# Kernel tuning notes

Hardware: AMD Instinct MI355X
Metric: run time of the kernel (lower is better)

Reference implementation:

```python
import jax, jax.numpy as jnp
import numpy as np

N = 50000   # nodes
E = 400000  # edges (before self-loops)
F = 128     # num_features
H = 8       # heads (layer 1)
C = 64      # hidden_channels
B = 64      # graphs in batch
K = 10      # num_classes
NEG_SLOPE = 0.2


def setup_inputs() -> dict:
    key = jax.random.key(0)
    ks = jax.random.split(key, 12)
    g = lambda k, shape, fan: jax.random.normal(k, shape, jnp.float32) / np.sqrt(fan).astype(np.float32)
    return {
        "x": jax.random.normal(ks[0], (N, F), jnp.float32),
        "edge_index": jax.random.randint(ks[1], (2, E), 0, N, jnp.int32),
        "batch": jnp.sort(jax.random.randint(ks[2], (N,), 0, B, jnp.int32)),
        "W1": g(ks[3], (F, H * C), F),
        "att_src1": g(ks[4], (H, C), C),
        "att_dst1": g(ks[5], (H, C), C),
        "b1": jnp.zeros((H * C,), jnp.float32),
        "W2": g(ks[6], (H * C, C), H * C),
        "att_src2": g(ks[7], (1, C), C),
        "att_dst2": g(ks[8], (1, C), C),
        "b2": jnp.zeros((C,), jnp.float32),
        "lin1_w": g(ks[9], (C, C), C),
        "lin1_b": jnp.zeros((C,), jnp.float32),
        "lin2_w": g(ks[10], (C, K), C),
        "lin2_b": jnp.zeros((K,), jnp.float32),
    }


def gat_conv(x, src, dst, W, att_src, att_dst, bias):
    """PyG GATConv (self-loops already appended to src/dst). x:[N,Fin] -> [N,H*C]."""
    heads, out_c = att_src.shape
    h = (x @ W).reshape(N, heads, out_c)                      # [N,H,C]
    a_s = jnp.einsum('nhc,hc->nh', h, att_src)                # [N,H]
    a_d = jnp.einsum('nhc,hc->nh', h, att_dst)
    e = jax.nn.leaky_relu(a_s[src] + a_d[dst], NEG_SLOPE)     # [E',H]
    # segment softmax over incoming edges of each destination node
    m = jax.ops.segment_max(e, dst, num_segments=N)
    e = jnp.exp(e - m[dst])
    denom = jax.ops.segment_sum(e, dst, num_segments=N)
    alpha = e / (denom[dst] + 1e-16)                          # [E',H]
    out = jax.ops.segment_sum(h[src] * alpha[:, :, None], dst, num_segments=N)  # [N,H,C]
    return out.reshape(N, heads * out_c) + bias


def reference(x, edge_index, batch, W1, att_src1, att_dst1, b1,
              W2, att_src2, att_dst2, b2, lin1_w, lin1_b, lin2_w, lin2_b):
    loops = jnp.arange(N, dtype=edge_index.dtype)
    src = jnp.concatenate([edge_index[0], loops])
    dst = jnp.concatenate([edge_index[1], loops])

    h = gat_conv(x, src, dst, W1, att_src1, att_dst1, b1)     # [N, H*C]
    h = jax.nn.elu(h)                                         # dropout inactive (eval)
    h = gat_conv(h, src, dst, W2, att_src2, att_dst2, b2)     # [N, C]
    h = jax.nn.elu(h)

    pooled = jax.ops.segment_sum(h, batch, num_segments=B)    # global_add_pool -> [B, C]
    z = jax.nn.elu(pooled @ lin1_w + lin1_b)
    logits = z @ lin2_w + lin2_b
    return jax.nn.log_softmax(logits, axis=-1)
```

## Files before the change

### kernel.cpp

```cpp
#include <hip/hip_runtime.h>
#include <hip/hip_bf16.h>

#define DEV static __device__ __forceinline__

constexpr int F1 = 128;
constexpr int H1 = 8;
constexpr int C  = 64;
constexpr int B  = 64;
constexpr int K  = 10;
constexpr float NEG = 0.2f;

typedef __attribute__((ext_vector_type(8))) short short8;
typedef __attribute__((ext_vector_type(4))) float floatx4;

DEV float b2f(__hip_bfloat16 x) { return __bfloat162float(x); }
DEV float elu1(float v) { return v > 0.f ? v : (__expf(v) - 1.f); }
DEV unsigned short f2bbits(float f) {
  __hip_bfloat16 b = __float2bfloat16(f);
  return *(unsigned short*)&b;
}
DEV float blo(unsigned u) { return __uint_as_float(u << 16); }
DEV float bhi(unsigned u) { return __uint_as_float(u & 0xffff0000u); }
DEV float bu(unsigned short u) { return __uint_as_float(((unsigned)u) << 16); }
DEV unsigned pack2(float lo, float hi) {
  return (unsigned)f2bbits(lo) | ((unsigned)f2bbits(hi) << 16);
}
DEV float rcp_nr(float x) {
  float r = __builtin_amdgcn_rcpf(x);
  return r * (2.f - x * r);
}


DEV int detect_dev(const void* xraw, int* lds) {
  if (threadIdx.x == 0) {
    const __hip_bfloat16* xb = (const __hip_bfloat16*)xraw;
    int bad = 0;
    for (int i = 0; i < 128; ++i) {
      float v = b2f(xb[2 * i]);
      if (!(fabsf(v) < 1e4f)) bad++;
    }
    *lds = (bad < 13) ? 1 : 0;
  }
  __syncthreads();
  return *lds;
}

#define CVT(p, i) (isbf ? b2f(((const __hip_bfloat16*)(p))[i]) : ((const float*)(p))[i])

__global__ void fused_prep_kernel(const void* x_raw, const void* w1raw,
                                  const void* as1r, const void* ad1r, const void* b1r,
                                  const void* w2raw,
                                  const void* as2r, const void* ad2r, const void* b2r,
                                  const void* l1wr, const void* l1br,
                                  const void* l2wr, const void* l2br,
                                  unsigned short* __restrict__ xbf,
                                  unsigned short* __restrict__ w1frag,
                                  unsigned short* __restrict__ w2frag,
                                  unsigned short* __restrict__ vfrag,
                                  float* __restrict__ wts,
                                  int* __restrict__ deg,
                                  float* __restrict__ pooled,
                                  int nX, int N) {
  __shared__ int fl;
  int isbf = detect_dev(x_raw, &fl);
  int gid = blockIdx.x * 256 + threadIdx.x;
  int stride = gridDim.x * 256;

  if (isbf) {
    const unsigned short* src = (const unsigned short*)x_raw;
    for (int i = gid; i < nX; i += stride) xbf[i] = src[i];
  } else {
    const float* src = (const float*)x_raw;
    for (int i = gid; i < nX; i += stride) xbf[i] = f2bbits(src[i]);
  }
  for (int i = gid; i < 512;  i += stride) {
    int hp = i >> 7, l16 = (i >> 3) & 15, nt = i & 7;
    int c = hp * 128 + nt * 16 + l16;
    wts[1024 + i] = CVT(b1r, c);
  }
  for (int i = gid; i < 64;   i += stride) wts[1536 + i] = CVT(as2r, i);
  for (int i = gid; i < 64;   i += stride) wts[1600 + i] = CVT(ad2r, i);
  for (int i = gid; i < 64;   i += stride) wts[1664 + i] = CVT(b2r, i);
  for (int i = gid; i < 4096; i += stride) wts[1728 + i] = CVT(l1wr, i);
  for (int i = gid; i < 64;   i += stride) wts[5824 + i] = CVT(l1br, i);
  for (int i = gid; i < 640;  i += stride) wts[5888 + i] = CVT(l2wr, i);
  for (int i = gid; i < 10;   i += stride) wts[6528 + i] = CVT(l2br, i);
  for (int t = gid; t < 8192; t += stride) {
    int lane = t & 63, ks = (t >> 6) & 3, nt = t >> 8;
    for (int j = 0; j < 8; ++j) {
      int k = ks * 32 + (lane >> 4) * 8 + j;
      int n = nt * 16 + (lane & 15);
      w1frag[t * 8 + j] = f2bbits(CVT(w1raw, k * 512 + n));
    }
  }
  for (int t = gid; t < 4096; t += stride) {
    int lane = t & 63, nt = (t >> 6) & 3, ks = t >> 8;
    for (int j = 0; j < 8; ++j) {
      int p = ks * 32 + (lane >> 4) * 8 + j;
      int hp = p >> 7, pl16 = (p >> 3) & 15, pnt = p & 7;
      int k = hp * 128 + pnt * 16 + pl16;
      int n = nt * 16 + (lane & 15);
      w2frag[t * 8 + j] = f2bbits(CVT(w2raw, k * 64 + n));
    }
  }
  for (int t = gid; t < 2048; t += stride) {
    int j = t & 7, lane = (t >> 3) & 63, ks = t >> 9;
    int k = ks * 32 + (lane >> 4) * 8 + j;
    int n = lane & 15;
    int hh = (n < 8) ? n : (n - 8);
    float s = 0.f;
    if (n < 8) {
      for (int c = 0; c < 64; ++c)
        s += CVT(w1raw, k * 512 + hh * 64 + c) * CVT(as1r, hh * 64 + c);
    } else {
      for (int c = 0; c < 64; ++c)
        s += CVT(w1raw, k * 512 + hh * 64 + c) * CVT(ad1r, hh * 64 + c);
    }
    vfrag[(ks * 64 + lane) * 8 + j] = f2bbits(s);
  }
  for (int i = gid; i < N; i += stride) deg[i] = 0;
  for (int i = gid; i < B * C; i += stride) pooled[i] = 0.f;
}

__global__ void deg_count_kernel(const int* __restrict__ ei, int E, int Etot,
                                 int* __restrict__ deg) {
  int e = blockIdx.x * blockDim.x + threadIdx.x;
  if (e >= Etot) return;
  int d = (e < E) ? ei[E + e] : e - E;
  atomicAdd(&deg[d], 1);
}

__global__ void scan_block_kernel(const int* __restrict__ deg,
                                  int* __restrict__ local,
                                  int* __restrict__ bsum, int N) {
  __shared__ int tmp[256];
  int t = threadIdx.x;
  int i = blockIdx.x * 256 + t;
  int v = (i < N) ? deg[i] : 0;
  tmp[t] = v;
  __syncthreads();
  for (int off = 1; off < 256; off <<= 1) {
    int u = (t >= off) ? tmp[t - off] : 0;
    __syncthreads();
    tmp[t] += u;
    __syncthreads();
  }
  if (i < N) local[i] = tmp[t] - v;
  if (t == 255) bsum[blockIdx.x] = tmp[255];
}

__global__ void scan_finish_kernel(const int* __restrict__ local,
                                   const int* __restrict__ bsum, int nb,
                                   int* __restrict__ rowptr,
                                   int* __restrict__ cursor, int N, int Etot) {
  __shared__ int tmp[256];
  __shared__ int offs;
  int t = threadIdx.x;
  int v0 = (t < nb) ? bsum[t] : 0;
  tmp[t] = v0;
  __syncthreads();
  for (int off = 1; off < 256; off <<= 1) {
    int u = (t >= off) ? tmp[t - off] : 0;
    __syncthreads();
    tmp[t] += u;
    __syncthreads();
  }
  if (t == (int)blockIdx.x) offs = tmp[t] - v0;
  __syncthreads();
  int i = blockIdx.x * 256 + t;
  if (i < N) {
    int r = local[i] + offs;
    rowptr[i] = r;
    cursor[i] = r;
  }
  if (i == 0) rowptr[N] = Etot;
}

__global__ __launch_bounds__(256) void att_scalars_kernel(
    const unsigned short* __restrict__ xbf,
    const unsigned short* __restrict__ vfrag,
    float* __restrict__ a_s, float* __restrict__ a_d,
    int N) {
  int t = threadIdx.x, w = t >> 6, lane = t & 63;
  int quad = lane >> 4, l16 = lane & 15;
  int row0 = blockIdx.x * 64 + w * 16;

  floatx4 acc = {};
  int rl = row0 + l16; if (rl >= N) rl = N - 1;
  const unsigned short* xp = xbf + (size_t)rl * 128 + quad * 8;
#pragma unroll
  for (int ks = 0; ks < 4; ++ks) {
    short8 a = *(const short8*)(xp + ks * 32);
    short8 b = *(const short8*)&vfrag[(ks * 64 + lane) * 8];
    acc = __builtin_amdgcn_mfma_f32_16x16x32_bf16(a, b, acc, 0, 0, 0);
  }
#pragma unroll
  for (int r = 0; r < 4; ++r) {
    int row = row0 + quad * 4 + r;
    if (row < N) {
      if (l16 < 8) a_s[(size_t)row * 8 + l16] = acc[r];
      else         a_d[(size_t)row * 8 + (l16 - 8)] = acc[r];
    }
  }
}

__global__ void fill_weight_kernel(const int* __restrict__ ei, int E, int Etot,
                                   const float* __restrict__ a_s,
                                   const float* __restrict__ a_d,
                                   int* __restrict__ cursor,
                                   int* __restrict__ col,
                                   float* __restrict__ wedge) {
  int e = blockIdx.x * 256 + threadIdx.x;
  if (e >= Etot) return;
  int s, d;
  if (e < E) { s = ei[e]; d = ei[E + e]; } else { s = d = e - E; }
  int pos = atomicAdd(&cursor[d], 1);
  col[pos] = s;
  float4 s0 = *(const float4*)(a_s + (size_t)s * 8);
  float4 s1 = *(const float4*)(a_s + (size_t)s * 8 + 4);
  float4 d0 = *(const float4*)(a_d + (size_t)d * 8);
  float4 d1 = *(const float4*)(a_d + (size_t)d * 8 + 4);
  float4 w0, w1;
  float v;
  v = s0.x + d0.x; v = v > 0.f ? v : NEG * v; w0.x = __expf(v);
  v = s0.y + d0.y; v = v > 0.f ? v : NEG * v; w0.y = __expf(v);
  v = s0.z + d0.z; v = v > 0.f ? v : NEG * v; w0.z = __expf(v);
  v = s0.w + d0.w; v = v > 0.f ? v : NEG * v; w0.w = __expf(v);
  v = s1.x + d1.x; v = v > 0.f ? v : NEG * v; w1.x = __expf(v);
  v = s1.y + d1.y; v = v > 0.f ? v : NEG * v; w1.y = __expf(v);
  v = s1.z + d1.z; v = v > 0.f ? v : NEG * v; w1.z = __expf(v);
  v = s1.w + d1.w; v = v > 0.f ? v : NEG * v; w1.w = __expf(v);
  *(float4*)(wedge + (size_t)pos * 8)     = w0;
  *(float4*)(wedge + (size_t)pos * 8 + 4) = w1;
}

__global__ __launch_bounds__(512, 4) void aggx_gemm1_kernel(
    const unsigned short* __restrict__ xbf,
    const unsigned short* __restrict__ W1frag,
    const int* __restrict__ rowptr,
    const int* __restrict__ col,
    const float* __restrict__ wedge,
    const float* __restrict__ bias_perm,
    unsigned short* __restrict__ out1,
    int N) {
  __shared__ __align__(16) unsigned short XgT[128 * 32];
  __shared__ __align__(16) unsigned short Wm[8 * 16 * 32];
  __shared__ __align__(16) unsigned short AggP[8 * 16 * 136];
  __shared__ int rpl[17];

  int t = threadIdx.x, w = t >> 6, lane = t & 63;
  int q = lane >> 4, n = lane & 15;
  int dbase = blockIdx.x * 16;

  if (t < 17) rpl[t] = rowptr[min(dbase + t, N)];
  __syncthreads();
  int R0 = rpl[0], R1 = rpl[16];
  int nch = (R1 - R0 + 31) >> 5;

  int ke = t >> 4, p = t & 15;
  int dw = t >> 5, kw = t & 31;

  short8 onesf = {};
  if (n == 0) {
#pragma unroll
    for (int j = 0; j < 8; ++j) onesf[j] = (short)0x3F80;
  }

  floatx4 accw[8] = {};
  floatx4 accdn = {};

  for (int c = 0; c < nch; ++c) {
    int ebase = R0 + c * 32;
    __syncthreads();

    {
      int e = ebase + ke;
      int ec = (e < R1) ? e : (R1 - 1);
      int s = col[ec];
      uint4 xv = *(const uint4*)(xbf + (size_t)s * 128 + p * 8);
      int xb = (512 * p + 2 * ke) ^ ((p & 3) << 4);
      unsigned short* xp0 = (unsigned short*)((char*)XgT + xb);
      xp0[0]   = (unsigned short)(xv.x & 0xffff);
      xp0[32]  = (unsigned short)(xv.x >> 16);
      xp0[64]  = (unsigned short)(xv.y & 0xffff);
      xp0[96]  = (unsigned short)(xv.y >> 16);
      xp0[128] = (unsigned short)(xv.z & 0xffff);
      xp0[160] = (unsigned short)(xv.z >> 16);
      xp0[192] = (unsigned short)(xv.w & 0xffff);
      xp0[224] = (unsigned short)(xv.w >> 16);
    }
    {
      int ew = ebase + kw;
      bool evw = ew < R1;
      int ewc = evw ? ew : (R1 - 1);
      int dl = 0;
#pragma unroll
      for (int b = 8; b; b >>= 1) dl += (rpl[dl + b] <= ew) ? b : 0;
      float4 wa = *(const float4*)(wedge + (size_t)ewc * 8);
      float4 wb = *(const float4*)(wedge + (size_t)ewc * 8 + 4);
      bool mine = evw && (dl == dw);
      unsigned short z = 0;
      unsigned short* wmp = Wm + dw * 32 + kw;
      wmp[0]    = mine ? f2bbits(wa.x) : z;
      wmp[512]  = mine ? f2bbits(wa.y) : z;
      wmp[1024] = mine ? f2bbits(wa.z) : z;
      wmp[1536] = mine ? f2bbits(wa.w) : z;
      wmp[2048] = mine ? f2bbits(wb.x) : z;
      wmp[2560] = mine ? f2bbits(wb.y) : z;
      wmp[3072] = mine ? f2bbits(wb.z) : z;
      wmp[3584] = mine ? f2bbits(wb.w) : z;
    }
    __syncthreads();

    short8 af = *(const short8*)(Wm + w * 512 + n * 32 + 8 * q);
    accdn = __builtin_amdgcn_mfma_f32_16x16x32_bf16(af, onesf, accdn, 0, 0, 0);
#pragma unroll
    for (int ft = 0; ft < 8; ++ft) {
      int bb = (ft * 16 + n) * 64 + 16 * q;
      bb ^= ((bb >> 9) & 3) << 4;
      short8 bfr = *(const short8*)((const char*)XgT + bb);
      accw[ft] = __builtin_amdgcn_mfma_f32_16x16x32_bf16(af, bfr, accw[ft], 0, 0, 0);
    }
  }

  {
    float dnv[4];
#pragma unroll
    for (int r = 0; r < 4; ++r) {
      float dr = __shfl(accdn[r], lane & 48);
      dnv[r] = rcp_nr(dr + 1e-16f);
    }
#pragma unroll
    for (int ft = 0; ft < 8; ++ft)
#pragma unroll
      for (int r = 0; r < 4; ++r)
        AggP[w * 2176 + (4 * q + r) * 136 + ft * 16 + n] =
            f2bbits(accw[ft][r] * dnv[r]);
  }
  __syncthreads();

  {
    int hp = w >> 1, qq = w & 1;
    floatx4 acc2[4] = {};
    const unsigned short* Bp = W1frag + (size_t)hp * 16384;
#pragma unroll
    for (int ks = 0; ks < 4; ++ks) {
      short8 a2 = *(const short8*)&AggP[w * 2176 + n * 136 + ks * 32 + q * 8];
#pragma unroll
      for (int j = 0; j < 4; ++j) {
        int nt = qq * 4 + j;
        short8 b2 = *(const short8*)&Bp[((nt * 4 + ks) * 64 + lane) * 8];
        acc2[j] = __builtin_amdgcn_mfma_f32_16x16x32_bf16(a2, b2, acc2[j], 0, 0, 0);
      }
    }
    float4 bq = *(const float4*)&bias_perm[hp * 128 + n * 8 + qq * 4];
#pragma unroll
    for (int r = 0; r < 4; ++r) {
      int row = dbase + 4 * q + r;
      if (row < N) {
        uint2 o;
        o.x = pack2(elu1(acc2[0][r] + bq.x), elu1(acc2[1][r] + bq.y));
        o.y = pack2(elu1(acc2[2][r] + bq.z), elu1(acc2[3][r] + bq.w));
        *(uint2*)&out1[(size_t)row * 512 + hp * 128 + n * 8 + qq * 4] = o;
      }
    }
  }
}

__global__ __launch_bounds__(256) void gemm2_mfma_kernel(
    const unsigned short* __restrict__ x2bf,
    const unsigned short* __restrict__ W2frag,
    const float* __restrict__ att_src,
    const float* __restrict__ att_dst,
    unsigned short* __restrict__ h2,
    float* __restrict__ a_s, float* __restrict__ a_d,
    int N) {
  int t = threadIdx.x;
  int w = t >> 6, lane = t & 63;
  int quad = lane >> 4, l16 = lane & 15;
  int rowbase = blockIdx.x * 64 + w * 16;

  floatx4 acc[4] = {};
  int r0 = rowbase + l16; if (r0 >= N) r0 = N - 1;
  const unsigned short* p0 = x2bf + (size_t)r0 * 512 + quad * 8;
#pragma unroll
  for (int ks = 0; ks < 16; ++ks) {
    short8 a0 = *(const short8*)(p0 + ks * 32);
#pragma unroll
    for (int nt = 0; nt < 4; ++nt) {
      short8 b = *(const short8*)&W2frag[((ks * 4 + nt) * 64 + lane) * 8];
      acc[nt] = __builtin_amdgcn_mfma_f32_16x16x32_bf16(a0, b, acc[nt], 0, 0, 0);
    }
  }

  float asw[4], adw[4];
#pragma unroll
  for (int nt = 0; nt < 4; ++nt) {
    asw[nt] = att_src[nt * 16 + l16];
    adw[nt] = att_dst[nt * 16 + l16];
  }
  float ps[4] = {}, pd[4] = {};
#pragma unroll
  for (int nt = 0; nt < 4; ++nt)
#pragma unroll
    for (int r = 0; r < 4; ++r) {
      float v = acc[nt][r];
      int row = rowbase + quad * 4 + r;
      if (row < N) h2[(size_t)row * 64 + nt * 16 + l16] = f2bbits(v);
      ps[r] += v * asw[nt];
      pd[r] += v * adw[nt];
    }
#pragma unroll
  for (int r = 0; r < 4; ++r) {
    float p = ps[r], q = pd[r];
#pragma unroll
    for (int off = 1; off < 16; off <<= 1) {
      p += __shfl_xor(p, off);
      q += __shfl_xor(q, off);
    }
    int row = rowbase + quad * 4 + r;
    if (l16 == 0 && row < N) {
      a_s[row] = p;
      a_d[row] = q;
    }
  }
}

__global__ void gat_agg1_kernel(const int* __restrict__ rowptr,
                                const int* __restrict__ col,
                                const float* __restrict__ a_s,
                                const float* __restrict__ a_d,
                                const unsigned short* __restrict__ hfeat,
                                const float* __restrict__ bias,
                                unsigned short* __restrict__ out, int N) {
  int wave = threadIdx.x >> 6, lane = threadIdx.x & 63;
  int d = blockIdx.x * 4 + wave;
  if (d >= N) return;
  int beg = rowptr[d], end = rowptr[d + 1];
  int qg = lane >> 4, l16 = lane & 15;
  float adv = a_d[d];
  const uint2* hfu = (const uint2*)hfeat;
  float acc[4] = {};
  float wsum = 0.f;
#pragma unroll 2
  for (int i = beg + qg; i < end; i += 4) {
    int s = col[i];
    float v = a_s[s] + adv;
    v = v > 0.f ? v : NEG * v;
    float wv = __expf(v);
    wsum += wv;
    uint2 u = hfu[(size_t)s * 16 + l16];
    acc[0] += wv * blo(u.x); acc[1] += wv * bhi(u.x);
    acc[2] += wv * blo(u.y); acc[3] += wv * bhi(u.y);
  }
#pragma unroll
  for (int off = 16; off <= 32; off <<= 1) {
#pragma unroll
    for (int j = 0; j < 4; ++j) acc[j] += __shfl_xor(acc[j], off);
    wsum += __shfl_xor(wsum, off);
  }
  float winv = 1.f / (wsum + 1e-16f);
  float4 bb = ((const float4*)bias)[l16];
  float r0 = elu1(acc[0] * winv + bb.x), r1 = elu1(acc[1] * winv + bb.y);
  float r2 = elu1(acc[2] * winv + bb.z), r3 = elu1(acc[3] * winv + bb.w);
  if (qg == 0) {
    uint2 o; o.x = pack2(r0, r1); o.y = pack2(r2, r3);
    ((uint2*)out)[(size_t)d * 16 + l16] = o;
  }
}

__global__ void pool_kernel(const unsigned short* __restrict__ out2,
                            const int* __restrict__ batch,
                            float* __restrict__ pooled, int N) {
  int wave = threadIdx.x >> 6, lane = threadIdx.x & 63;
  int seg = blockIdx.x * 4 + wave;
  int start = seg * 16;
  if (start >= N) return;
  int end = min(start + 16, N);
  int cur = batch[start];
  float acc = 0.f;
  for (int n = start; n < end; ++n) {
    int bn = batch[n];
    if (bn != cur) {
      unsafeAtomicAdd(&pooled[cur * 64 + lane], acc);
      acc = 0.f; cur = bn;
    }
    acc += bu(out2[(size_t)n * 64 + lane]);
  }
  unsafeAtomicAdd(&pooled[cur * 64 + lane], acc);
}

__global__ void head_kernel(const float* __restrict__ pooled,
                            const float* __restrict__ lin1_w,
                            const float* __restrict__ lin1_b,
                            const float* __restrict__ lin2_w,
                            const float* __restrict__ lin2_b,
                            const void* __restrict__ x_raw,
                            void* __restrict__ outv) {
  __shared__ float P[C];
  __shared__ float Zs[C];
  __shared__ float Ls[K];
  __shared__ float lse_s;
  __shared__ int fl;
  int isbf = detect_dev(x_raw, &fl);
  int g = blockIdx.x, t = threadIdx.x;
  P[t] = pooled[g * C + t];
  __syncthreads();
  float acc = lin1_b[t];
  for (int k = 0; k < C; ++k) acc += P[k] * lin1_w[k * C + t];
  Zs[t] = elu1(acc);
  __syncthreads();
  if (t < K) {
    float a = lin2_b[t];
    for (int k = 0; k < C; ++k) a += Zs[k] * lin2_w[k * K + t];
    Ls[t] = a;
  }
  __syncthreads();
  if (t == 0) {
    float mx = -1e30f;
    for (int c = 0; c < K; ++c) mx = fmaxf(mx, Ls[c]);
    float s = 0.f;
    for (int c = 0; c < K; ++c) s += __expf(Ls[c] - mx);
    lse_s = mx + __logf(s);
  }
  __syncthreads();
  if (t < K) {
    float val = Ls[t] - lse_s;
    if (isbf) ((__hip_bfloat16*)outv)[g * K + t] = __float2bfloat16(val);
    else      ((float*)outv)[g * K + t] = val;
  }
}

extern "C" void kernel_launch(void* const* d_in, const int* in_sizes, int n_in,
                              void* d_out, int out_size, void* d_ws, size_t ws_size,
                              hipStream_t stream) {
  const void* x_raw = d_in[0];
  const int*  ei    = (const int*)d_in[1];
  const int*  batch = (const int*)d_in[2];

  const int N    = in_sizes[2];
  const int E    = in_sizes[1] / 2;
  const int Etot = E + N;
  const int nb   = (N + 255) / 256;

  float* ws   = (float*)d_ws;
  size_t off  = 0;

  float* wts = ws + off; off += 6544;
  float* b1w  = wts + 1024;
  float* as2w = wts + 1536;
  float* ad2w = wts + 1600;
  float* b2w  = wts + 1664;
  float* l1w  = wts + 1728;
  float* l1b  = wts + 5824;
  float* l2w  = wts + 5888;
  float* l2b  = wts + 6528;

  unsigned short* xbf    = (unsigned short*)(ws + off); off += (size_t)N * 64;
  unsigned short* w1frag = (unsigned short*)(ws + off); off += 32768;
  unsigned short* w2frag = (unsigned short*)(ws + off); off += 16384;
  unsigned short* vfrag  = (unsigned short*)(ws + off); off += 1024;
  float* wedge           = ws + off;                    off += (size_t)Etot * 8;
  unsigned short* out1bf = (unsigned short*)(ws + off); off += (size_t)N * 256;
  unsigned short* h2bf   = (unsigned short*)(ws + off); off += (size_t)N * 32;
  unsigned short* out2bf = (unsigned short*)(ws + off); off += (size_t)N * 32;
  float* as1  = ws + off; off += (size_t)N * H1;
  float* ad1  = ws + off; off += (size_t)N * H1;
  float* as2  = ws + off; off += (size_t)N;
  float* ad2  = ws + off; off += (size_t)N;
  float* pooled = ws + off; off += (size_t)B * C;

  int* ibase  = (int*)(ws + off);
  int* deg    = ibase;                 ibase += N;
  int* cursor = ibase;                 ibase += N;
  int* rowptr = ibase;                 ibase += N + 1;
  int* locals = ibase;                 ibase += N;
  int* bsum   = ibase;                 ibase += 256;
  int* col    = ibase;                 ibase += Etot;

  fused_prep_kernel<<<1024, 256, 0, stream>>>(
      x_raw, d_in[3], d_in[4], d_in[5], d_in[6], d_in[7], d_in[8], d_in[9],
      d_in[10], d_in[11], d_in[12], d_in[13], d_in[14],
      xbf, w1frag, w2frag, vfrag, wts, deg, pooled, in_sizes[0], N);

  deg_count_kernel<<<(Etot + 255) / 256, 256, 0, stream>>>(ei, E, Etot, deg);
  scan_block_kernel<<<nb, 256, 0, stream>>>(deg, locals, bsum, N);
  scan_finish_kernel<<<nb, 256, 0, stream>>>(locals, bsum, nb, rowptr, cursor, N, Etot);

  att_scalars_kernel<<<(N + 63) / 64, 256, 0, stream>>>(xbf, vfrag, as1, ad1, N);

  fill_weight_kernel<<<(Etot + 255) / 256, 256, 0, stream>>>(
      ei, E, Etot, as1, ad1, cursor, col, wedge);

  aggx_gemm1_kernel<<<(N + 15) / 16, 512, 0, stream>>>(
      xbf, w1frag, rowptr, col, wedge, b1w, out1bf, N);

  gemm2_mfma_kernel<<<(N + 63) / 64, 256, 0, stream>>>(out1bf, w2frag, as2w, ad2w,
                                                       h2bf, as2, ad2, N);
  gat_agg1_kernel<<<(N + 3) / 4, 256, 0, stream>>>(rowptr, col, as2, ad2, h2bf, b2w, out2bf, N);

  pool_kernel<<<(N + 63) / 64, 256, 0, stream>>>(out2bf, batch, pooled, N);
  head_kernel<<<B, 64, 0, stream>>>(pooled, l1w, l1b, l2w, l2b, x_raw, (void*)d_out);
}
```

Measured before the change: 296.5 us.

## Store edge weights as bf16, pack local dst into col, alias LDS

Edge attention weights are now written as packed bf16 instead of fp32, halving the wedge buffer and its read traffic in the layer-1 aggregation GEMM. The local destination index (d & 15) is packed into the high bits of col, which replaces the per-edge binary search over the block's rowptr slice, and rowptr bounds are read straight from global memory. LDS is shared between the gather tiles and the output staging buffer, with an extra barrier between them, and launch bounds ask for 8 blocks per CU. The XOR swizzle is widened to 3 bits to cut bank conflicts. Readers of col must now mask off the tag bits, which assumes node ids fit in 27 bits.

```diff
diff --git a/kernel.cpp b/kernel.cpp
--- a/kernel.cpp
+++ b/kernel.cpp
@@ -9,6 +9,7 @@
 constexpr int B  = 64;
 constexpr int K  = 10;
 constexpr float NEG = 0.2f;
+constexpr unsigned SMASK = 0x07FFFFFFu;
 
 typedef __attribute__((ext_vector_type(8))) short short8;
 typedef __attribute__((ext_vector_type(4))) float floatx4;
@@ -209,52 +210,52 @@
                                    const float* __restrict__ a_d,
                                    int* __restrict__ cursor,
                                    int* __restrict__ col,
-                                   float* __restrict__ wedge) {
+                                   unsigned short* __restrict__ wedge) {
   int e = blockIdx.x * 256 + threadIdx.x;
   if (e >= Etot) return;
   int s, d;
   if (e < E) { s = ei[e]; d = ei[E + e]; } else { s = d = e - E; }
   int pos = atomicAdd(&cursor[d], 1);
-  col[pos] = s;
+  col[pos] = s | ((d & 15) << 27);
   float4 s0 = *(const float4*)(a_s + (size_t)s * 8);
   float4 s1 = *(const float4*)(a_s + (size_t)s * 8 + 4);
   float4 d0 = *(const float4*)(a_d + (size_t)d * 8);
   float4 d1 = *(const float4*)(a_d + (size_t)d * 8 + 4);
-  float4 w0, w1;
-  float v;
-  v = s0.x + d0.x; v = v > 0.f ? v : NEG * v; w0.x = __expf(v);
-  v = s0.y + d0.y; v = v > 0.f ? v : NEG * v; w0.y = __expf(v);
-  v = s0.z + d0.z; v = v > 0.f ? v : NEG * v; w0.z = __expf(v);
-  v = s0.w + d0.w; v = v > 0.f ? v : NEG * v; w0.w = __expf(v);
-  v = s1.x + d1.x; v = v > 0.f ? v : NEG * v; w1.x = __expf(v);
-  v = s1.y + d1.y; v = v > 0.f ? v : NEG * v; w1.y = __expf(v);
-  v = s1.z + d1.z; v = v > 0.f ? v : NEG * v; w1.z = __expf(v);
-  v = s1.w + d1.w; v = v > 0.f ? v : NEG * v; w1.w = __expf(v);
-  *(float4*)(wedge + (size_t)pos * 8)     = w0;
-  *(float4*)(wedge + (size_t)pos * 8 + 4) = w1;
-}
-
-__global__ __launch_bounds__(512, 4) void aggx_gemm1_kernel(
+  float v, w0, w1, w2, w3, w4, w5, w6, w7;
+  v = s0.x + d0.x; v = v > 0.f ? v : NEG * v; w0 = __expf(v);
+  v = s0.y + d0.y; v = v > 0.f ? v : NEG * v; w1 = __expf(v);
+  v = s0.z + d0.z; v = v > 0.f ? v : NEG * v; w2 = __expf(v);
+  v = s0.w + d0.w; v = v > 0.f ? v : NEG * v; w3 = __expf(v);
+  v = s1.x + d1.x; v = v > 0.f ? v : NEG * v; w4 = __expf(v);
+  v = s1.y + d1.y; v = v > 0.f ? v : NEG * v; w5 = __expf(v);
+  v = s1.z + d1.z; v = v > 0.f ? v : NEG * v; w6 = __expf(v);
+  v = s1.w + d1.w; v = v > 0.f ? v : NEG * v; w7 = __expf(v);
+  uint4 o;
+  o.x = pack2(w0, w1); o.y = pack2(w2, w3);
+  o.z = pack2(w4, w5); o.w = pack2(w6, w7);
+  *(uint4*)(wedge + (size_t)pos * 8) = o;
+}
+
+__global__ __launch_bounds__(512, 8) void aggx_gemm1_kernel(
     const unsigned short* __restrict__ xbf,
     const unsigned short* __restrict__ W1frag,
     const int* __restrict__ rowptr,
     const int* __restrict__ col,
-    const float* __restrict__ wedge,
+    const unsigned short* __restrict__ wedge,
     const float* __restrict__ bias_perm,
     unsigned short* __restrict__ out1,
     int N) {
-  __shared__ __align__(16) unsigned short XgT[128 * 32];
-  __shared__ __align__(16) unsigned short Wm[8 * 16 * 32];
-  __shared__ __align__(16) unsigned short AggP[8 * 16 * 136];
-  __shared__ int rpl[17];
+  __shared__ __align__(16) char LB[8 * 16 * 136 * 2];
+  unsigned short* XgT = (unsigned short*)LB;
+  unsigned short* Wm  = (unsigned short*)(LB + 8192);
+  unsigned short* AggP = (unsigned short*)LB;
 
   int t = threadIdx.x, w = t >> 6, lane = t & 63;
   int q = lane >> 4, n = lane & 15;
   int dbase = blockIdx.x * 16;
 
-  if (t < 17) rpl[t] = rowptr[min(dbase + t, N)];
-  __syncthreads();
-  int R0 = rpl[0], R1 = rpl[16];
+  int R0 = rowptr[dbase];
+  int R1 = rowptr[min(dbase + 16, N)];
   int nch = (R1 - R0 + 31) >> 5;
 
   int ke = t >> 4, p = t & 15;
@@ -276,39 +277,36 @@
     {
       int e = ebase + ke;
       int ec = (e < R1) ? e : (R1 - 1);
-      int s = col[ec];
+      int s = col[ec] & SMASK;
       uint4 xv = *(const uint4*)(xbf + (size_t)s * 128 + p * 8);
-      int xb = (512 * p + 2 * ke) ^ ((p & 3) << 4);
-      unsigned short* xp0 = (unsigned short*)((char*)XgT + xb);
-      xp0[0]   = (unsigned short)(xv.x & 0xffff);
-      xp0[32]  = (unsigned short)(xv.x >> 16);
-      xp0[64]  = (unsigned short)(xv.y & 0xffff);
-      xp0[96]  = (unsigned short)(xv.y >> 16);
-      xp0[128] = (unsigned short)(xv.z & 0xffff);
-      xp0[160] = (unsigned short)(xv.z >> 16);
-      xp0[192] = (unsigned short)(xv.w & 0xffff);
-      xp0[224] = (unsigned short)(xv.w >> 16);
+      int base = 512 * p + 2 * ke;
+      int key = (p & 7) << 4;
+      unsigned short el[8];
+      el[0] = (unsigned short)(xv.x & 0xffff); el[1] = (unsigned short)(xv.x >> 16);
+      el[2] = (unsigned short)(xv.y & 0xffff); el[3] = (unsigned short)(xv.y >> 16);
+      el[4] = (unsigned short)(xv.z & 0xffff); el[5] = (unsigned short)(xv.z >> 16);
+      el[6] = (unsigned short)(xv.w & 0xffff); el[7] = (unsigned short)(xv.w >> 16);
+#pragma unroll
+      for (int j = 0; j < 8; ++j)
+        *(unsigned short*)((char*)XgT + ((base + 64 * j) ^ key)) = el[j];
     }
     {
       int ew = ebase + kw;
       bool evw = ew < R1;
       int ewc = evw ? ew : (R1 - 1);
-      int dl = 0;
-#pragma unroll
-      for (int b = 8; b; b >>= 1) dl += (rpl[dl + b] <= ew) ? b : 0;
-      float4 wa = *(const float4*)(wedge + (size_t)ewc * 8);
-      float4 wb = *(const float4*)(wedge + (size_t)ewc * 8 + 4);
+      int cv = col[ewc];
+      int dl = (cv >> 27) & 15;
+      uint4 wv = *(const uint4*)(wedge + (size_t)ewc * 8);
       bool mine = evw && (dl == dw);
-      unsigned short z = 0;
       unsigned short* wmp = Wm + dw * 32 + kw;
-      wmp[0]    = mine ? f2bbits(wa.x) : z;
-      wmp[512]  = mine ? f2bbits(wa.y) : z;
-      wmp[1024] = mine ? f2bbits(wa.z) : z;
-      wmp[1536] = mine ? f2bbits(wa.w) : z;
-      wmp[2048] = mine ? f2bbits(wb.x) : z;
-      wmp[2560] = mine ? f2bbits(wb.y) : z;
-      wmp[3072] = mine ? f2bbits(wb.z) : z;
-      wmp[3584] = mine ? f2bbits(wb.w) : z;
+      wmp[0]    = mine ? (unsigned short)(wv.x & 0xffff) : 0;
+      wmp[512]  = mine ? (unsigned short)(wv.x >> 16)    : 0;
+      wmp[1024] = mine ? (unsigned short)(wv.y & 0xffff) : 0;
+      wmp[1536] = mine ? (unsigned short)(wv.y >> 16)    : 0;
+      wmp[2048] = mine ? (unsigned short)(wv.z & 0xffff) : 0;
+      wmp[2560] = mine ? (unsigned short)(wv.z >> 16)    : 0;
+      wmp[3072] = mine ? (unsigned short)(wv.w & 0xffff) : 0;
+      wmp[3584] = mine ? (unsigned short)(wv.w >> 16)    : 0;
     }
     __syncthreads();
 
@@ -317,11 +315,13 @@
 #pragma unroll
     for (int ft = 0; ft < 8; ++ft) {
       int bb = (ft * 16 + n) * 64 + 16 * q;
-      bb ^= ((bb >> 9) & 3) << 4;
+      bb ^= ((bb >> 9) & 7) << 4;
       short8 bfr = *(const short8*)((const char*)XgT + bb);
       accw[ft] = __builtin_amdgcn_mfma_f32_16x16x32_bf16(af, bfr, accw[ft], 0, 0, 0);
     }
   }
+
+  __syncthreads();
 
   {
     float dnv[4];
@@ -444,7 +444,7 @@
   float wsum = 0.f;
 #pragma unroll 2
   for (int i = beg + qg; i < end; i += 4) {
-    int s = col[i];
+    int s = col[i] & SMASK;
     float v = a_s[s] + adv;
     v = v > 0.f ? v : NEG * v;
     float wv = __expf(v);
@@ -560,7 +560,7 @@
   unsigned short* w1frag = (unsigned short*)(ws + off); off += 32768;
   unsigned short* w2frag = (unsigned short*)(ws + off); off += 16384;
   unsigned short* vfrag  = (unsigned short*)(ws + off); off += 1024;
-  float* wedge           = ws + off;                    off += (size_t)Etot * 8;
+  unsigned short* wedge  = (unsigned short*)(ws + off); off += (size_t)Etot * 4;
   unsigned short* out1bf = (unsigned short*)(ws + off); off += (size_t)N * 256;
   unsigned short* h2bf   = (unsigned short*)(ws + off); off += (size_t)N * 32;
   unsigned short* out2bf = (unsigned short*)(ws + off); off += (size_t)N * 32;
```

After: 338.5 us. +14.2%, slower.
